# Kernel optimization log

Hardware: AMD Instinct MI355X
Metric: run time of the kernel (lower is better)

Reference implementation:

```python
import jax, jax.numpy as jnp
import numpy as np

N = 50000       # nodes
E = 800000      # edges (avg degree 16)
D_IN = 128      # input_dim
H = 256         # hidden_dim
Z = H // 2      # 128, latent / conv3-4 width
D_OUT = 64      # output_dim


def _glorot(key, shape):
    fan_in, fan_out = shape
    lim = float(np.sqrt(6.0 / (fan_in + fan_out)))
    return jax.random.uniform(key, shape, jnp.float32, -lim, lim)


def setup_inputs() -> dict:
    key = jax.random.key(0)
    ks = jax.random.split(key, 16)
    inp = {
        "x": jax.random.uniform(ks[0], (N, D_IN), jnp.float32),
        "edge_index": jax.random.randint(ks[1], (2, E), 0, N, jnp.int32),
        "epsilon": jax.random.normal(ks[2], (N, Z), jnp.float32),
        # SAGEConv params: Wl (neighbor/aggr path, with bias), Wr (root path, no bias)
        "Wl1": _glorot(ks[3], (D_IN, H)), "bl1": jnp.zeros((H,), jnp.float32), "Wr1": _glorot(ks[4], (D_IN, H)),
        "Wl2": _glorot(ks[5], (H, H)),    "bl2": jnp.zeros((H,), jnp.float32), "Wr2": _glorot(ks[6], (H, H)),
        "Wl3": _glorot(ks[7], (Z, Z)),    "bl3": jnp.zeros((Z,), jnp.float32), "Wr3": _glorot(ks[8], (Z, Z)),
        "Wl4": _glorot(ks[9], (Z, Z)),    "bl4": jnp.zeros((Z,), jnp.float32), "Wr4": _glorot(ks[10], (Z, Z)),
        "W_lin": _glorot(ks[11], (Z, D_OUT)), "b_lin": jnp.zeros((D_OUT,), jnp.float32),
    }
    return inp


def _sage_conv(x, src, dst, Wl, bl, Wr):
    # PyG SAGEConv (mean aggr): out = lin_l(mean_{j in N(i)} x_j) + lin_r(x_i)
    msg = x[src]                                             # [E, d] gather
    agg = jax.ops.segment_sum(msg, dst, num_segments=N)      # [N, d]
    cnt = jax.ops.segment_sum(jnp.ones((src.shape[0],), x.dtype), dst, num_segments=N)
    mean = agg / jnp.maximum(cnt, 1.0)[:, None]
    return mean @ Wl + bl + x @ Wr


def reference(x, edge_index, epsilon,
              Wl1, bl1, Wr1, Wl2, bl2, Wr2,
              Wl3, bl3, Wr3, Wl4, bl4, Wr4,
              W_lin, b_lin):
    src, dst = edge_index[0], edge_index[1]
    h = x / 1000.0 - 0.5
    h = jnp.sin(_sage_conv(h, src, dst, Wl1, bl1, Wr1))      # [N, H]
    h = _sage_conv(h, src, dst, Wl2, bl2, Wr2)               # [N, H]
    mean = h[:, :Z]
    log_var = h[:, Z:]
    z = mean + jnp.exp(log_var) * epsilon                    # reparameterize
    h = jax.nn.relu(_sage_conv(z, src, dst, Wl3, bl3, Wr3))
    h = jax.nn.relu(_sage_conv(h, src, dst, Wl4, bl4, Wr4))
    out = jax.nn.sigmoid(h @ W_lin + b_lin) * 1000.0
    return out, mean, log_var
```

## Files before the change

kernel.cpp:

```cpp
#include <hip/hip_runtime.h>
#include <hip/hip_bf16.h>

#define N_NODES 50000
#define E_EDGES 800000

using u16 = unsigned short;
typedef short bf8 __attribute__((ext_vector_type(8)));
typedef float f32x4 __attribute__((ext_vector_type(4)));

__device__ __forceinline__ float bf2f(u16 h) {
    union { unsigned u; float f; } v;
    v.u = ((unsigned)h) << 16;
    return v.f;
}
__device__ __forceinline__ u16 f2bf(float f) {
    union { float f; unsigned u; } v;
    v.f = f;
    unsigned r = v.u + 0x7FFF + ((v.u >> 16) & 1);
    return (u16)(r >> 16);
}

struct WtArgs {
    const float* src[9];
    u16* dst[9];
    int K[9];
    int N[9];
};

__global__ __launch_bounds__(256) void k_wpack(WtArgs a) {
    int wi = blockIdx.y;
    int K = a.K[wi], NC = a.N[wi];
    int KS = K / 32;
    int chunks = (NC / 16) * KS * 64;
    for (int c = blockIdx.x * 256 + threadIdx.x; c < chunks;
         c += gridDim.x * 256) {
        int l = c & 63;
        int rest = c >> 6;
        int ks = rest % KS, gni = rest / KS;
        int n = gni * 16 + (l & 15);
        int kb = ks * 32 + (l >> 4) * 8;
        u16 outv[8];
#pragma unroll
        for (int j = 0; j < 8; ++j)
            outv[j] = f2bf(a.src[wi][(size_t)(kb + j) * NC + n]);
        *(bf8*)&a.dst[wi][(size_t)c * 8] = *(bf8*)outv;
    }
}

__global__ __launch_bounds__(256) void k_prep(const float* __restrict__ x,
                                              u16* __restrict__ h0) {
    int total = N_NODES * 128 / 4;
    for (int i = blockIdx.x * 256 + threadIdx.x; i < total;
         i += gridDim.x * 256) {
        float4 v = *(const float4*)(x + (size_t)i * 4);
        ushort4 o;
        o.x = f2bf(v.x * 0.001f - 0.5f);
        o.y = f2bf(v.y * 0.001f - 0.5f);
        o.z = f2bf(v.z * 0.001f - 0.5f);
        o.w = f2bf(v.w * 0.001f - 0.5f);
        *(ushort4*)(h0 + (size_t)i * 4) = o;
    }
}

__global__ void k_count(const int* __restrict__ dst, int* __restrict__ deg) {
    for (int i = blockIdx.x * blockDim.x + threadIdx.x; i < E_EDGES;
         i += gridDim.x * blockDim.x)
        atomicAdd(&deg[dst[i]], 1);
}

#define SCAN_B 49

__global__ __launch_bounds__(1024) void k_scan1(const int* __restrict__ deg,
                                                int* __restrict__ bsum) {
    __shared__ int sm[1024];
    int i = blockIdx.x * 1024 + threadIdx.x;
    sm[threadIdx.x] = (i < N_NODES) ? deg[i] : 0;
    __syncthreads();
    for (int ofs = 512; ofs > 0; ofs >>= 1) {
        if (threadIdx.x < ofs) sm[threadIdx.x] += sm[threadIdx.x + ofs];
        __syncthreads();
    }
    if (threadIdx.x == 0) bsum[blockIdx.x] = sm[0];
}

__global__ void k_scan2(const int* __restrict__ bsum, int* __restrict__ bofs) {
    int l = threadIdx.x;
    int v = (l < SCAN_B) ? bsum[l] : 0;
    int orig = v;
    for (int d = 1; d < 64; d <<= 1) {
        int u = __shfl_up(v, d, 64);
        if (l >= d) v += u;
    }
    if (l < SCAN_B) bofs[l] = v - orig;
}

__global__ __launch_bounds__(1024) void k_scan3(const int* __restrict__ deg,
                                                const int* __restrict__ bofs,
                                                int* __restrict__ rowptr,
                                                float* __restrict__ dinv) {
    __shared__ int sm[1024];
    int i = blockIdx.x * 1024 + threadIdx.x;
    int d = (i < N_NODES) ? deg[i] : 0;
    sm[threadIdx.x] = d;
    __syncthreads();
    for (int ofs = 1; ofs < 1024; ofs <<= 1) {
        int u = (threadIdx.x >= (unsigned)ofs) ? sm[threadIdx.x - ofs] : 0;
        __syncthreads();
        sm[threadIdx.x] += u;
        __syncthreads();
    }
    if (i < N_NODES) {
        int incl = sm[threadIdx.x] + bofs[blockIdx.x];
        rowptr[i] = incl - d;
        dinv[i] = 1.0f / fmaxf((float)d, 1.0f);
        if (i == N_NODES - 1) rowptr[N_NODES] = incl;
    }
}

__global__ void k_fill(const int* __restrict__ src, const int* __restrict__ dst,
                       const int* __restrict__ rowptr, int* __restrict__ cursor,
                       int* __restrict__ colidx) {
    for (int i = blockIdx.x * blockDim.x + threadIdx.x; i < E_EDGES;
         i += gridDim.x * blockDim.x) {
        int d = dst[i];
        int pos = rowptr[d] + atomicAdd(&cursor[d], 1);
        colidx[pos] = src[i];
    }
}

template <int D>
__global__ __launch_bounds__(256) void k_aggregate(
    const u16* __restrict__ h, const int* __restrict__ rowptr,
    const int* __restrict__ colidx, const float* __restrict__ dinv,
    u16* __restrict__ mean) {
    constexpr int VA = D / 16;
    int node = (int)((blockIdx.x * 256 + threadIdx.x) >> 6);
    int lane = threadIdx.x & 63;
    if (node >= N_NODES) return;
    int sub = lane >> 4, lr = lane & 15;
    int beg = rowptr[node], end = rowptr[node + 1];
    float acc[VA] = {};
    int e = beg + sub;
    for (; e + 4 < end; e += 8) {
        int s0 = colidx[e];
        int s1 = colidx[e + 4];
        const u16* p0 = h + (size_t)s0 * D + lr * VA;
        const u16* p1 = h + (size_t)s1 * D + lr * VA;
        bf8 r0 = *(const bf8*)p0;
        bf8 r1 = *(const bf8*)p1;
        if (VA == 16) {
            bf8 r0b = *(const bf8*)(p0 + 8);
            bf8 r1b = *(const bf8*)(p1 + 8);
#pragma unroll
            for (int j = 0; j < 8; ++j) {
                acc[j] += bf2f((u16)r0[j]) + bf2f((u16)r1[j]);
                acc[8 + j] += bf2f((u16)r0b[j]) + bf2f((u16)r1b[j]);
            }
        } else {
#pragma unroll
            for (int j = 0; j < 8; ++j)
                acc[j] += bf2f((u16)r0[j]) + bf2f((u16)r1[j]);
        }
    }
    for (; e < end; e += 4) {
        int s = colidx[e];
        const u16* row = h + (size_t)s * D + lr * VA;
        bf8 r0 = *(const bf8*)row;
#pragma unroll
        for (int j = 0; j < 8; ++j) acc[j] += bf2f((u16)r0[j]);
        if (VA == 16) {
            bf8 r1 = *(const bf8*)(row + 8);
#pragma unroll
            for (int j = 0; j < 8; ++j) acc[8 + j] += bf2f((u16)r1[j]);
        }
    }
#pragma unroll
    for (int j = 0; j < VA; ++j) {
        acc[j] += __shfl_xor(acc[j], 16);
        acc[j] += __shfl_xor(acc[j], 32);
    }
    if (sub == 0) {
        float inv = dinv[node];
        u16 outv[VA];
#pragma unroll
        for (int j = 0; j < VA; ++j) outv[j] = f2bf(acc[j] * inv);
        u16* o = mean + (size_t)node * D + lr * VA;
        *(bf8*)o = *(bf8*)&outv[0];
        if (VA == 16) *(bf8*)(o + 8) = *(bf8*)&outv[8];
    }
}

enum { ACT_NONE = 0, ACT_SIN = 1, ACT_RELU = 2, ACT_SIGMOID1000 = 3, ACT_VAE = 4 };

template <int K, int NCB, int NC, int YS, int ACT, bool OUT_F32, bool TWO_PASS>
__global__ __launch_bounds__(512) void k_gemm(
    const u16* __restrict__ A1, const u16* __restrict__ Wp1,
    const u16* __restrict__ A2, const u16* __restrict__ Wp2,
    const float* __restrict__ bias, void* __restrict__ Cout,
    float* __restrict__ out_mean, float* __restrict__ out_lv,
    const float* __restrict__ eps) {
    constexpr int M = N_NODES;
    constexpr int NG = NCB / 16;
    constexpr int KS = K / 32;
    constexpr int CHUNKS = NG * KS * 64;
    constexpr int GX = (M / 16 + 7) / 8;
    constexpr int NWG = ((GX * YS + 7) / 8) * 8;
    constexpr int CPX = NWG / 8;
    extern __shared__ char smem[];
    u16* Bs = (u16*)smem;

    const int bid = blockIdx.x;
    const int wid = (bid & 7) * CPX + (bid >> 3);
    const int x = wid / YS;
    const int y = wid % YS;
    if (x >= GX) return;

    const int t = threadIdx.x;
    const int lane = t & 63;
    const int wave = t >> 6;
    const int lr = lane & 15;
    const int sub = lane >> 4;
    const int row0 = (x * 8 + wave) * 16;
    const int arow = row0 + lr;
    const bool rowOK = arow < M;

    auto mapGroup = [&](int ni) {
        if (ACT == ACT_VAE)
            return ni < NG / 2 ? y * (NG / 2) + ni
                               : (NC / 32) + y * (NG / 2) + (ni - NG / 2);
        return y * NG + ni;
    };

    f32x4 acc[NG];
#pragma unroll
    for (int i = 0; i < NG; ++i) acc[i] = (f32x4){0.f, 0.f, 0.f, 0.f};

    auto stageW = [&](const u16* __restrict__ Wp) {
#pragma unroll
        for (int i = 0; i < CHUNKS / 512; ++i) {
            int c = t + i * 512;
            int l = c & 63;
            int ks = (c >> 6) % KS;
            int ni = c / (64 * KS);
            size_t gsrc = ((size_t)mapGroup(ni) * KS + ks) * 64 + l;
            *(bf8*)&Bs[(size_t)c * 8] = *(const bf8*)(Wp + gsrc * 8);
        }
    };

    auto pass = [&](const u16* __restrict__ A, const u16* __restrict__ Wp) {
        stageW(Wp);
        __syncthreads();
        const u16* ap = A + (size_t)arow * K + sub * 8;
#pragma unroll
        for (int ks = 0; ks < KS; ++ks) {
            bf8 a = {0, 0, 0, 0, 0, 0, 0, 0};
            if (rowOK) a = *(const bf8*)(ap + ks * 32);
#pragma unroll
            for (int ni = 0; ni < NG; ++ni) {
                bf8 b = *(const bf8*)&Bs[(((size_t)ni * KS + ks) * 64 + lane) * 8];
                acc[ni] =
                    __builtin_amdgcn_mfma_f32_16x16x32_bf16(a, b, acc[ni], 0, 0, 0);
            }
        }
        __syncthreads();
    };

    pass(A1, Wp1);
    if (TWO_PASS) pass(A2, Wp2);

    if (ACT == ACT_VAE) {
#pragma unroll
        for (int ni = 0; ni < NG / 2; ++ni) {
            int colm = y * (NCB / 2) + ni * 16 + lr;
            float bm = bias[colm];
            float bl = bias[colm + 128];
#pragma unroll
            for (int r = 0; r < 4; ++r) {
                int row = row0 + sub * 4 + r;
                if (row >= M) continue;
                float mv = acc[ni][r] + bm;
                float lv = acc[ni + NG / 2][r] + bl;
                size_t o = (size_t)row * 128 + colm;
                out_mean[o] = mv;
                out_lv[o] = lv;
                ((u16*)Cout)[o] = f2bf(mv + __expf(lv) * eps[o]);
            }
        }
    } else {
#pragma unroll
        for (int ni = 0; ni < NG; ++ni) {
            int col = y * NCB + ni * 16 + lr;
            float bv = bias[col];
#pragma unroll
            for (int r = 0; r < 4; ++r) {
                int row = row0 + sub * 4 + r;
                if (row >= M) continue;
                float v = acc[ni][r] + bv;
                if (ACT == ACT_SIN) v = __sinf(v);
                else if (ACT == ACT_RELU) v = fmaxf(v, 0.f);
                else if (ACT == ACT_SIGMOID1000) v = 1000.f / (1.f + __expf(-v));
                if (OUT_F32)
                    ((float*)Cout)[(size_t)row * NC + col] = v;
                else
                    ((u16*)Cout)[(size_t)row * NC + col] = f2bf(v);
            }
        }
    }
}

extern "C" void kernel_launch(void* const* d_in, const int* in_sizes, int n_in,
                              void* d_out, int out_size, void* d_ws,
                              size_t ws_size, hipStream_t stream) {
    const int N = N_NODES;
    const float* x = (const float*)d_in[0];
    const int* ei = (const int*)d_in[1];
    const float* eps = (const float*)d_in[2];
    const float* Wl1 = (const float*)d_in[3];
    const float* bl1 = (const float*)d_in[4];
    const float* Wr1 = (const float*)d_in[5];
    const float* Wl2 = (const float*)d_in[6];
    const float* bl2 = (const float*)d_in[7];
    const float* Wr2 = (const float*)d_in[8];
    const float* Wl3 = (const float*)d_in[9];
    const float* bl3 = (const float*)d_in[10];
    const float* Wr3 = (const float*)d_in[11];
    const float* Wl4 = (const float*)d_in[12];
    const float* bl4 = (const float*)d_in[13];
    const float* Wr4 = (const float*)d_in[14];
    const float* W_lin = (const float*)d_in[15];
    const float* b_lin = (const float*)d_in[16];

    const int* src = ei;
    const int* dst = ei + E_EDGES;

    char* w = (char*)d_ws;
    auto alloc = [&](size_t b) {
        void* p = (void*)w;
        w += (b + 255) & ~(size_t)255;
        return p;
    };
    int* deg = (int*)alloc((size_t)N * 4);
    int* rowptr = (int*)alloc((size_t)(N + 1) * 4);
    int* cursor = (int*)alloc((size_t)N * 4);
    int* colidx = (int*)alloc((size_t)E_EDGES * 4);
    float* dinv = (float*)alloc((size_t)N * 4);
    int* bsum = (int*)alloc(64 * 4);
    int* bofs = (int*)alloc(64 * 4);
    u16* hbA = (u16*)alloc((size_t)N * 256 * 2);
    u16* hbB = (u16*)alloc((size_t)N * 256 * 2);
    u16* hbC = (u16*)alloc((size_t)N * 256 * 2);
    static const int wK[9] = {128, 128, 256, 256, 128, 128, 128, 128, 128};
    static const int wN[9] = {256, 256, 256, 256, 128, 128, 128, 128, 64};
    u16* Wt[9];
    for (int i = 0; i < 9; ++i) Wt[i] = (u16*)alloc((size_t)wK[i] * wN[i] * 2);

    float* out_final = (float*)d_out;
    float* out_mean = out_final + (size_t)N * 64;
    float* out_lv = out_mean + (size_t)N * 128;

    hipMemsetAsync(deg, 0, (size_t)N * 4, stream);
    hipMemsetAsync(cursor, 0, (size_t)N * 4, stream);

    WtArgs wa;
    const float* wsrc[9] = {Wl1, Wr1, Wl2, Wr2, Wl3, Wr3, Wl4, Wr4, W_lin};
    for (int i = 0; i < 9; ++i) {
        wa.src[i] = wsrc[i];
        wa.dst[i] = Wt[i];
        wa.K[i] = wK[i];
        wa.N[i] = wN[i];
    }
    k_wpack<<<dim3(32, 9), 256, 0, stream>>>(wa);

    k_prep<<<2048, 256, 0, stream>>>(x, hbA);
    k_count<<<3125, 256, 0, stream>>>(dst, deg);
    k_scan1<<<SCAN_B, 1024, 0, stream>>>(deg, bsum);
    k_scan2<<<1, 64, 0, stream>>>(bsum, bofs);
    k_scan3<<<SCAN_B, 1024, 0, stream>>>(deg, bofs, rowptr, dinv);
    k_fill<<<3125, 256, 0, stream>>>(src, dst, rowptr, cursor, colidx);

    const int aggBlocks = (N * 64 + 255) / 256;
    auto nwg = [](int YS) { return ((391 * YS + 7) / 8) * 8; };
    auto shm = [](int NCB, int K) { return (size_t)NCB * K * 2; };

    k_aggregate<128><<<aggBlocks, 256, 0, stream>>>(hbA, rowptr, colidx, dinv,
                                                    hbB);
    k_gemm<128, 128, 256, 2, ACT_SIN, false, true>
        <<<nwg(2), 512, shm(128, 128), stream>>>(hbB, Wt[0], hbA, Wt[1], bl1,
                                                 hbC, nullptr, nullptr, nullptr);

    k_aggregate<256><<<aggBlocks, 256, 0, stream>>>(hbC, rowptr, colidx, dinv,
                                                    hbB);
    k_gemm<256, 64, 256, 4, ACT_VAE, false, true>
        <<<nwg(4), 512, shm(64, 256), stream>>>(hbB, Wt[2], hbC, Wt[3], bl2,
                                                hbA, out_mean, out_lv, eps);

    k_aggregate<128><<<aggBlocks, 256, 0, stream>>>(hbA, rowptr, colidx, dinv,
                                                    hbB);
    k_gemm<128, 64, 128, 2, ACT_RELU, false, true>
        <<<nwg(2), 512, shm(64, 128), stream>>>(hbB, Wt[4], hbA, Wt[5], bl3,
                                                hbC, nullptr, nullptr, nullptr);

    k_aggregate<128><<<aggBlocks, 256, 0, stream>>>(hbC, rowptr, colidx, dinv,
                                                    hbB);
    k_gemm<128, 64, 128, 2, ACT_RELU, false, true>
        <<<nwg(2), 512, shm(64, 128), stream>>>(hbB, Wt[6], hbC, Wt[7], bl4,
                                                hbA, nullptr, nullptr, nullptr);

    k_gemm<128, 32, 64, 2, ACT_SIGMOID1000, true, false>
        <<<nwg(2), 512, shm(32, 128), stream>>>(hbA, Wt[8], nullptr, nullptr,
                                                b_lin, out_final, nullptr,
                                                nullptr, nullptr);
}
```

Measured before the change: 371.4 us.

## Compute two row tiles per wave in GEMM and unroll aggregation gather by four

The GEMM kernel now has each wave compute two 16-row MFMA tiles that share the same B fragments from LDS, halving the workgroup count and reusing staged weights across more rows. The first layer's GEMM is retiled to 64-column blocks with four column groups. The aggregation loop processes four neighbors per iteration instead of two, putting more independent gathers in flight. These add register pressure from doubled accumulators and may reduce occupancy.

Result: slower. 379.5 us (+2.2%).

```diff
diff --git a/kernel.cpp b/kernel.cpp
--- a/kernel.cpp
+++ b/kernel.cpp
@@ -141,25 +141,28 @@
     int beg = rowptr[node], end = rowptr[node + 1];
     float acc[VA] = {};
     int e = beg + sub;
-    for (; e + 4 < end; e += 8) {
-        int s0 = colidx[e];
-        int s1 = colidx[e + 4];
-        const u16* p0 = h + (size_t)s0 * D + lr * VA;
-        const u16* p1 = h + (size_t)s1 * D + lr * VA;
+    for (; e + 12 < end; e += 16) {
+        const u16* p0 = h + (size_t)colidx[e] * D + lr * VA;
+        const u16* p1 = h + (size_t)colidx[e + 4] * D + lr * VA;
+        const u16* p2 = h + (size_t)colidx[e + 8] * D + lr * VA;
+        const u16* p3 = h + (size_t)colidx[e + 12] * D + lr * VA;
         bf8 r0 = *(const bf8*)p0;
         bf8 r1 = *(const bf8*)p1;
+        bf8 r2 = *(const bf8*)p2;
+        bf8 r3 = *(const bf8*)p3;
+#pragma unroll
+        for (int j = 0; j < 8; ++j)
+            acc[j] += (bf2f((u16)r0[j]) + bf2f((u16)r1[j])) +
+                      (bf2f((u16)r2[j]) + bf2f((u16)r3[j]));
         if (VA == 16) {
-            bf8 r0b = *(const bf8*)(p0 + 8);
-            bf8 r1b = *(const bf8*)(p1 + 8);
-#pragma unroll
-            for (int j = 0; j < 8; ++j) {
-                acc[j] += bf2f((u16)r0[j]) + bf2f((u16)r1[j]);
-                acc[8 + j] += bf2f((u16)r0b[j]) + bf2f((u16)r1b[j]);
-            }
-        } else {
+            bf8 s0 = *(const bf8*)(p0 + 8);
+            bf8 s1 = *(const bf8*)(p1 + 8);
+            bf8 s2 = *(const bf8*)(p2 + 8);
+            bf8 s3 = *(const bf8*)(p3 + 8);
 #pragma unroll
             for (int j = 0; j < 8; ++j)
-                acc[j] += bf2f((u16)r0[j]) + bf2f((u16)r1[j]);
+                acc[8 + j] += (bf2f((u16)s0[j]) + bf2f((u16)s1[j])) +
+                              (bf2f((u16)s2[j]) + bf2f((u16)s3[j]));
         }
     }
     for (; e < end; e += 4) {
@@ -203,7 +206,7 @@
     constexpr int NG = NCB / 16;
     constexpr int KS = K / 32;
     constexpr int CHUNKS = NG * KS * 64;
-    constexpr int GX = (M / 16 + 7) / 8;
+    constexpr int GX = (M + 255) / 256;
     constexpr int NWG = ((GX * YS + 7) / 8) * 8;
     constexpr int CPX = NWG / 8;
     extern __shared__ char smem[];
@@ -220,9 +223,11 @@
     const int wave = t >> 6;
     const int lr = lane & 15;
     const int sub = lane >> 4;
-    const int row0 = (x * 8 + wave) * 16;
-    const int arow = row0 + lr;
-    const bool rowOK = arow < M;
+    const int wrow0 = (x * 8 + wave) * 32;
+    const int arow0 = wrow0 + lr;
+    const int arow1 = wrow0 + 16 + lr;
+    const bool ok0 = arow0 < M;
+    const bool ok1 = arow1 < M;
 
     auto mapGroup = [&](int ni) {
         if (ACT == ACT_VAE)
@@ -231,9 +236,12 @@
         return y * NG + ni;
     };
 
-    f32x4 acc[NG];
-#pragma unroll
-    for (int i = 0; i < NG; ++i) acc[i] = (f32x4){0.f, 0.f, 0.f, 0.f};
+    f32x4 acc0[NG], acc1[NG];
+#pragma unroll
+    for (int i = 0; i < NG; ++i) {
+        acc0[i] = (f32x4){0.f, 0.f, 0.f, 0.f};
+        acc1[i] = (f32x4){0.f, 0.f, 0.f, 0.f};
+    }
 
     auto stageW = [&](const u16* __restrict__ Wp) {
 #pragma unroll
@@ -250,16 +258,21 @@
     auto pass = [&](const u16* __restrict__ A, const u16* __restrict__ Wp) {
         stageW(Wp);
         __syncthreads();
-        const u16* ap = A + (size_t)arow * K + sub * 8;
+        const u16* ap0 = A + (size_t)arow0 * K + sub * 8;
+        const u16* ap1 = A + (size_t)arow1 * K + sub * 8;
 #pragma unroll
         for (int ks = 0; ks < KS; ++ks) {
-            bf8 a = {0, 0, 0, 0, 0, 0, 0, 0};
-            if (rowOK) a = *(const bf8*)(ap + ks * 32);
+            bf8 a0 = {0, 0, 0, 0, 0, 0, 0, 0};
+            bf8 a1 = {0, 0, 0, 0, 0, 0, 0, 0};
+            if (ok0) a0 = *(const bf8*)(ap0 + ks * 32);
+            if (ok1) a1 = *(const bf8*)(ap1 + ks * 32);
 #pragma unroll
             for (int ni = 0; ni < NG; ++ni) {
                 bf8 b = *(const bf8*)&Bs[(((size_t)ni * KS + ks) * 64 + lane) * 8];
-                acc[ni] =
-                    __builtin_amdgcn_mfma_f32_16x16x32_bf16(a, b, acc[ni], 0, 0, 0);
+                acc0[ni] =
+                    __builtin_amdgcn_mfma_f32_16x16x32_bf16(a0, b, acc0[ni], 0, 0, 0);
+                acc1[ni] =
+                    __builtin_amdgcn_mfma_f32_16x16x32_bf16(a1, b, acc1[ni], 0, 0, 0);
             }
         }
         __syncthreads();
@@ -275,15 +288,19 @@
             float bm = bias[colm];
             float bl = bias[colm + 128];
 #pragma unroll
-            for (int r = 0; r < 4; ++r) {
-                int row = row0 + sub * 4 + r;
-                if (row >= M) continue;
-                float mv = acc[ni][r] + bm;
-                float lv = acc[ni + NG / 2][r] + bl;
-                size_t o = (size_t)row * 128 + colm;
-                out_mean[o] = mv;
-                out_lv[o] = lv;
-                ((u16*)Cout)[o] = f2bf(mv + __expf(lv) * eps[o]);
+            for (int s = 0; s < 2; ++s) {
+#pragma unroll
+                for (int r = 0; r < 4; ++r) {
+                    int row = wrow0 + s * 16 + sub * 4 + r;
+                    if (row >= M) continue;
+                    float mv = (s ? acc1[ni][r] : acc0[ni][r]) + bm;
+                    float lv =
+                        (s ? acc1[ni + NG / 2][r] : acc0[ni + NG / 2][r]) + bl;
+                    size_t o = (size_t)row * 128 + colm;
+                    out_mean[o] = mv;
+                    out_lv[o] = lv;
+                    ((u16*)Cout)[o] = f2bf(mv + __expf(lv) * eps[o]);
+                }
             }
         }
     } else {
@@ -292,17 +309,21 @@
             int col = y * NCB + ni * 16 + lr;
             float bv = bias[col];
 #pragma unroll
-            for (int r = 0; r < 4; ++r) {
-                int row = row0 + sub * 4 + r;
-                if (row >= M) continue;
-                float v = acc[ni][r] + bv;
-                if (ACT == ACT_SIN) v = __sinf(v);
-                else if (ACT == ACT_RELU) v = fmaxf(v, 0.f);
-                else if (ACT == ACT_SIGMOID1000) v = 1000.f / (1.f + __expf(-v));
-                if (OUT_F32)
-                    ((float*)Cout)[(size_t)row * NC + col] = v;
-                else
-                    ((u16*)Cout)[(size_t)row * NC + col] = f2bf(v);
+            for (int s = 0; s < 2; ++s) {
+#pragma unroll
+                for (int r = 0; r < 4; ++r) {
+                    int row = wrow0 + s * 16 + sub * 4 + r;
+                    if (row >= M) continue;
+                    float v = (s ? acc1[ni][r] : acc0[ni][r]) + bv;
+                    if (ACT == ACT_SIN) v = __sinf(v);
+                    else if (ACT == ACT_RELU) v = fmaxf(v, 0.f);
+                    else if (ACT == ACT_SIGMOID1000)
+                        v = 1000.f / (1.f + __expf(-v));
+                    if (OUT_F32)
+                        ((float*)Cout)[(size_t)row * NC + col] = v;
+                    else
+                        ((u16*)Cout)[(size_t)row * NC + col] = f2bf(v);
+                }
             }
         }
     }
@@ -379,14 +400,14 @@
     k_fill<<<3125, 256, 0, stream>>>(src, dst, rowptr, cursor, colidx);
 
     const int aggBlocks = (N * 64 + 255) / 256;
-    auto nwg = [](int YS) { return ((391 * YS + 7) / 8) * 8; };
+    auto nwg = [](int YS) { return ((196 * YS + 7) / 8) * 8; };
     auto shm = [](int NCB, int K) { return (size_t)NCB * K * 2; };
 
     k_aggregate<128><<<aggBlocks, 256, 0, stream>>>(hbA, rowptr, colidx, dinv,
                                                     hbB);
-    k_gemm<128, 128, 256, 2, ACT_SIN, false, true>
-        <<<nwg(2), 512, shm(128, 128), stream>>>(hbB, Wt[0], hbA, Wt[1], bl1,
-                                                 hbC, nullptr, nullptr, nullptr);
+    k_gemm<128, 64, 256, 4, ACT_SIN, false, true>
+        <<<nwg(4), 512, shm(64, 128), stream>>>(hbB, Wt[0], hbA, Wt[1], bl1,
+                                                hbC, nullptr, nullptr, nullptr);
 
     k_aggregate<256><<<aggBlocks, 256, 0, stream>>>(hbC, rowptr, colidx, dinv,
                                                     hbB);
```

## Stage both weight passes via async global-to-LDS loads and prefetch A fragments

Applied to the files above, without the earlier changes.

The GEMM kernel now loads both weight matrices into shared memory up front with global_load_lds direct-to-LDS transfers and a single barrier, instead of two staged passes through registers each with its own syncs. The K loop is merged across the two passes and software-prefetches the next A fragment. The VAE epsilon values are loaded before the main loop, and layer 1 switches to a narrower column split with twice as many workgroups. Doubling LDS per block may reduce occupancy.

After: 367.3 us. Within noise of the previous version (-1.1%).

```diff
diff --git a/kernel.cpp b/kernel.cpp
--- a/kernel.cpp
+++ b/kernel.cpp
@@ -19,6 +19,11 @@
     unsigned r = v.u + 0x7FFF + ((v.u >> 16) & 1);
     return (u16)(r >> 16);
 }
+
+#define GLOAD_LDS16(gsrc, ldst)                                            \
+    __builtin_amdgcn_global_load_lds(                                      \
+        (const __attribute__((address_space(1))) void*)(gsrc),             \
+        (__attribute__((address_space(3))) void*)(ldst), 16, 0, 0)
 
 struct WtArgs {
     const float* src[9];
@@ -201,8 +206,9 @@
     const float* __restrict__ eps) {
     constexpr int M = N_NODES;
     constexpr int NG = NCB / 16;
-    constexpr int KS = K / 32;
-    constexpr int CHUNKS = NG * KS * 64;
+    constexpr int KS1 = K / 32;
+    constexpr int KST = TWO_PASS ? 2 * KS1 : KS1;
+    constexpr int CH1 = NG * KS1 * 64;
     constexpr int GX = (M / 16 + 7) / 8;
     constexpr int NWG = ((GX * YS + 7) / 8) * 8;
     constexpr int CPX = NWG / 8;
@@ -231,42 +237,78 @@
         return y * NG + ni;
     };
 
+    {
+#pragma unroll
+        for (int i = 0; i < CH1 / 512; ++i) {
+            int c = t + i * 512;
+            int ks = (c >> 6) % KS1;
+            int ni = c / (64 * KS1);
+            const u16* gsrc =
+                Wp1 + (((size_t)mapGroup(ni) * KS1 + ks) * 64 + lane) * 8;
+            u16* ldst = Bs + ((size_t)(i * 512 + wave * 64)) * 8;
+            GLOAD_LDS16(gsrc, ldst);
+        }
+        if (TWO_PASS) {
+#pragma unroll
+            for (int i = 0; i < CH1 / 512; ++i) {
+                int c = t + i * 512;
+                int ks = (c >> 6) % KS1;
+                int ni = c / (64 * KS1);
+                const u16* gsrc =
+                    Wp2 + (((size_t)mapGroup(ni) * KS1 + ks) * 64 + lane) * 8;
+                u16* ldst = Bs + ((size_t)(CH1 + i * 512 + wave * 64)) * 8;
+                GLOAD_LDS16(gsrc, ldst);
+            }
+        }
+    }
+
+    float epsv[ACT == ACT_VAE ? 8 : 1];
+    if (ACT == ACT_VAE) {
+#pragma unroll
+        for (int ni = 0; ni < NG / 2; ++ni) {
+#pragma unroll
+            for (int r = 0; r < 4; ++r) {
+                int row = row0 + sub * 4 + r;
+                int colm = y * (NCB / 2) + ni * 16 + lr;
+                epsv[ni * 4 + r] =
+                    (row < M) ? eps[(size_t)row * 128 + colm] : 0.f;
+            }
+        }
+    }
+
     f32x4 acc[NG];
 #pragma unroll
     for (int i = 0; i < NG; ++i) acc[i] = (f32x4){0.f, 0.f, 0.f, 0.f};
 
-    auto stageW = [&](const u16* __restrict__ Wp) {
-#pragma unroll
-        for (int i = 0; i < CHUNKS / 512; ++i) {
-            int c = t + i * 512;
-            int l = c & 63;
-            int ks = (c >> 6) % KS;
-            int ni = c / (64 * KS);
-            size_t gsrc = ((size_t)mapGroup(ni) * KS + ks) * 64 + l;
-            *(bf8*)&Bs[(size_t)c * 8] = *(const bf8*)(Wp + gsrc * 8);
-        }
+    auto aptr = [&](int ks) {
+        return (ks < KS1 ? A1 + (size_t)arow * K + ks * 32
+                         : A2 + (size_t)arow * K + (ks - KS1) * 32) +
+               sub * 8;
     };
 
-    auto pass = [&](const u16* __restrict__ A, const u16* __restrict__ Wp) {
-        stageW(Wp);
-        __syncthreads();
-        const u16* ap = A + (size_t)arow * K + sub * 8;
-#pragma unroll
-        for (int ks = 0; ks < KS; ++ks) {
-            bf8 a = {0, 0, 0, 0, 0, 0, 0, 0};
-            if (rowOK) a = *(const bf8*)(ap + ks * 32);
-#pragma unroll
-            for (int ni = 0; ni < NG; ++ni) {
-                bf8 b = *(const bf8*)&Bs[(((size_t)ni * KS + ks) * 64 + lane) * 8];
-                acc[ni] =
-                    __builtin_amdgcn_mfma_f32_16x16x32_bf16(a, b, acc[ni], 0, 0, 0);
-            }
-        }
-        __syncthreads();
-    };
-
-    pass(A1, Wp1);
-    if (TWO_PASS) pass(A2, Wp2);
+    __syncthreads();
+
+    bf8 acur = {0, 0, 0, 0, 0, 0, 0, 0};
+    if (rowOK) acur = *(const bf8*)aptr(0);
+#pragma unroll
+    for (int ks = 0; ks < KST; ++ks) {
+        bf8 anext = {0, 0, 0, 0, 0, 0, 0, 0};
+        if (ks + 1 < KST && rowOK) anext = *(const bf8*)aptr(ks + 1);
+#pragma unroll
+        for (int ni = 0; ni < NG; ++ni) {
+            bf8 b = *(const bf8*)&Bs[(((size_t)ks * NG + 0) * 0 +
+                                      ((ks < KS1)
+                                           ? (((size_t)ni * KS1 + ks) * 64)
+                                           : ((size_t)CH1 +
+                                              ((size_t)ni * KS1 + (ks - KS1)) *
+                                                  64)) +
+                                      lane) *
+                                     8];
+            acc[ni] =
+                __builtin_amdgcn_mfma_f32_16x16x32_bf16(acur, b, acc[ni], 0, 0, 0);
+        }
+        acur = anext;
+    }
 
     if (ACT == ACT_VAE) {
 #pragma unroll
@@ -283,7 +325,7 @@
                 size_t o = (size_t)row * 128 + colm;
                 out_mean[o] = mv;
                 out_lv[o] = lv;
-                ((u16*)Cout)[o] = f2bf(mv + __expf(lv) * eps[o]);
+                ((u16*)Cout)[o] = f2bf(mv + __expf(lv) * epsv[ni * 4 + r]);
             }
         }
     } else {
@@ -380,30 +422,30 @@
 
     const int aggBlocks = (N * 64 + 255) / 256;
     auto nwg = [](int YS) { return ((391 * YS + 7) / 8) * 8; };
-    auto shm = [](int NCB, int K) { return (size_t)NCB * K * 2; };
+    auto shm = [](int NCB, int Ktot) { return (size_t)NCB * Ktot * 2; };
 
     k_aggregate<128><<<aggBlocks, 256, 0, stream>>>(hbA, rowptr, colidx, dinv,
                                                     hbB);
-    k_gemm<128, 128, 256, 2, ACT_SIN, false, true>
-        <<<nwg(2), 512, shm(128, 128), stream>>>(hbB, Wt[0], hbA, Wt[1], bl1,
-                                                 hbC, nullptr, nullptr, nullptr);
+    k_gemm<128, 64, 256, 4, ACT_SIN, false, true>
+        <<<nwg(4), 512, shm(64, 256), stream>>>(hbB, Wt[0], hbA, Wt[1], bl1,
+                                                hbC, nullptr, nullptr, nullptr);
 
     k_aggregate<256><<<aggBlocks, 256, 0, stream>>>(hbC, rowptr, colidx, dinv,
                                                     hbB);
     k_gemm<256, 64, 256, 4, ACT_VAE, false, true>
-        <<<nwg(4), 512, shm(64, 256), stream>>>(hbB, Wt[2], hbC, Wt[3], bl2,
+        <<<nwg(4), 512, shm(64, 512), stream>>>(hbB, Wt[2], hbC, Wt[3], bl2,
                                                 hbA, out_mean, out_lv, eps);
 
     k_aggregate<128><<<aggBlocks, 256, 0, stream>>>(hbA, rowptr, colidx, dinv,
                                                     hbB);
     k_gemm<128, 64, 128, 2, ACT_RELU, false, true>
-        <<<nwg(2), 512, shm(64, 128), stream>>>(hbB, Wt[4], hbA, Wt[5], bl3,
+        <<<nwg(2), 512, shm(64, 256), stream>>>(hbB, Wt[4], hbA, Wt[5], bl3,
                                                 hbC, nullptr, nullptr, nullptr);
 
     k_aggregate<128><<<aggBlocks, 256, 0, stream>>>(hbC, rowptr, colidx, dinv,
                                                     hbB);
     k_gemm<128, 64, 128, 2, ACT_RELU, false, true>
-        <<<nwg(2), 512, shm(64, 128), stream>>>(hbB, Wt[6], hbC, Wt[7], bl4,
+        <<<nwg(2), 512, shm(64, 256), stream>>>(hbB, Wt[6], hbC, Wt[7], bl4,
                                                 hbA, nullptr, nullptr, nullptr);
 
     k_gemm<128, 32, 64, 2, ACT_SIGMOID1000, true, false>
```

## Co-schedule root-path GEMM with neighbor aggregation in one heterogeneous launch

Applied to the files above, without the earlier changes.

Each SAGE layer's root-path GEMM (x @ Wr) now runs inside the aggregation kernel. Every R-th block does a GEMM tile and writes a bf16 partial S, while the other blocks do the mean aggregation, so compute-bound MFMA work can overlap the memory-bound gather. The second kernel then does only the mean @ Wl GEMM and adds S in its epilogue. Weight staging also switches to global_load_lds direct-to-LDS copies, and the A operand gets a one-step register prefetch. The costs are an extra round trip through a bf16 S buffer, an added rounding step for the root term, and block-interleaving ratios that were tuned by hand.

Result: slower. 384.3 us (+3.5%).

```diff
diff --git a/kernel.cpp b/kernel.cpp
--- a/kernel.cpp
+++ b/kernel.cpp
@@ -19,6 +19,11 @@
     unsigned r = v.u + 0x7FFF + ((v.u >> 16) & 1);
     return (u16)(r >> 16);
 }
+
+#define GLOAD_LDS16(gsrc, ldst)                                            \
+    __builtin_amdgcn_global_load_lds(                                      \
+        (const __attribute__((address_space(1))) void*)(gsrc),             \
+        (__attribute__((address_space(3))) void*)(ldst), 16, 0, 0)
 
 struct WtArgs {
     const float* src[9];
@@ -128,24 +133,98 @@
     }
 }
 
-template <int D>
-__global__ __launch_bounds__(256) void k_aggregate(
-    const u16* __restrict__ h, const int* __restrict__ rowptr,
-    const int* __restrict__ colidx, const float* __restrict__ dinv,
-    u16* __restrict__ mean) {
-    constexpr int VA = D / 16;
-    int node = (int)((blockIdx.x * 256 + threadIdx.x) >> 6);
-    int lane = threadIdx.x & 63;
-    if (node >= N_NODES) return;
-    int sub = lane >> 4, lr = lane & 15;
+template <int K, int NCB, int NC, int YS, int R>
+__global__ __launch_bounds__(512) void k_conv_a(
+    const u16* __restrict__ H, const u16* __restrict__ Wp,
+    const int* __restrict__ rowptr, const int* __restrict__ colidx,
+    const float* __restrict__ dinv, u16* __restrict__ meanOut,
+    u16* __restrict__ S) {
+    constexpr int M = N_NODES;
+    constexpr int NG = NCB / 16;
+    constexpr int KS = K / 32;
+    constexpr int CH = NG * KS * 64;
+    constexpr int GX = (M / 16 + 7) / 8;
+    constexpr int GEMM_B = ((GX * YS + 7) / 8) * 8;
+    constexpr int CPX = GEMM_B / 8;
+    extern __shared__ char smem[];
+    u16* Bs = (u16*)smem;
+
+    const int bid = blockIdx.x;
+    const int t = threadIdx.x;
+    const int lane = t & 63;
+    const int wave = t >> 6;
+    const int lr = lane & 15;
+    const int sub = lane >> 4;
+
+    if (bid % R == R - 1) {
+        const int gid = bid / R;
+        const int wid = (gid & 7) * CPX + (gid >> 3);
+        const int x = wid / YS;
+        const int y = wid % YS;
+        if (x >= GX) return;
+        const int row0 = (x * 8 + wave) * 16;
+        const int arow = row0 + lr;
+        const bool rowOK = arow < M;
+
+#pragma unroll
+        for (int i = 0; i < CH / 512; ++i) {
+            int c = t + i * 512;
+            int ks = (c >> 6) % KS;
+            int ni = c / (64 * KS);
+            const u16* gsrc =
+                Wp + (((size_t)(y * NG + ni) * KS + ks) * 64 + lane) * 8;
+            u16* ldst = Bs + ((size_t)(i * 512 + wave * 64)) * 8;
+            GLOAD_LDS16(gsrc, ldst);
+        }
+
+        f32x4 acc[NG];
+#pragma unroll
+        for (int i = 0; i < NG; ++i) acc[i] = (f32x4){0.f, 0.f, 0.f, 0.f};
+
+        const u16* ap = H + (size_t)arow * K + sub * 8;
+        __syncthreads();
+
+        bf8 acur = {0, 0, 0, 0, 0, 0, 0, 0};
+        if (rowOK) acur = *(const bf8*)ap;
+#pragma unroll
+        for (int ks = 0; ks < KS; ++ks) {
+            bf8 anext = {0, 0, 0, 0, 0, 0, 0, 0};
+            if (ks + 1 < KS && rowOK) anext = *(const bf8*)(ap + (ks + 1) * 32);
+#pragma unroll
+            for (int ni = 0; ni < NG; ++ni) {
+                bf8 b =
+                    *(const bf8*)&Bs[(((size_t)ni * KS + ks) * 64 + lane) * 8];
+                acc[ni] = __builtin_amdgcn_mfma_f32_16x16x32_bf16(acur, b,
+                                                                  acc[ni], 0, 0, 0);
+            }
+            acur = anext;
+        }
+
+#pragma unroll
+        for (int ni = 0; ni < NG; ++ni) {
+            int col = y * NCB + ni * 16 + lr;
+#pragma unroll
+            for (int r = 0; r < 4; ++r) {
+                int row = row0 + sub * 4 + r;
+                if (row >= M) continue;
+                S[(size_t)row * NC + col] = f2bf(acc[ni][r]);
+            }
+        }
+        return;
+    }
+
+    constexpr int VA = K / 16;
+    const int agg_id = bid - bid / R;
+    const int node = agg_id * 8 + wave;
+    if (node >= M) return;
     int beg = rowptr[node], end = rowptr[node + 1];
     float acc[VA] = {};
     int e = beg + sub;
     for (; e + 4 < end; e += 8) {
         int s0 = colidx[e];
         int s1 = colidx[e + 4];
-        const u16* p0 = h + (size_t)s0 * D + lr * VA;
-        const u16* p1 = h + (size_t)s1 * D + lr * VA;
+        const u16* p0 = H + (size_t)s0 * K + lr * VA;
+        const u16* p1 = H + (size_t)s1 * K + lr * VA;
         bf8 r0 = *(const bf8*)p0;
         bf8 r1 = *(const bf8*)p1;
         if (VA == 16) {
@@ -164,7 +243,7 @@
     }
     for (; e < end; e += 4) {
         int s = colidx[e];
-        const u16* row = h + (size_t)s * D + lr * VA;
+        const u16* row = H + (size_t)s * K + lr * VA;
         bf8 r0 = *(const bf8*)row;
 #pragma unroll
         for (int j = 0; j < 8; ++j) acc[j] += bf2f((u16)r0[j]);
@@ -184,7 +263,7 @@
         u16 outv[VA];
 #pragma unroll
         for (int j = 0; j < VA; ++j) outv[j] = f2bf(acc[j] * inv);
-        u16* o = mean + (size_t)node * D + lr * VA;
+        u16* o = meanOut + (size_t)node * K + lr * VA;
         *(bf8*)o = *(bf8*)&outv[0];
         if (VA == 16) *(bf8*)(o + 8) = *(bf8*)&outv[8];
     }
@@ -192,20 +271,19 @@
 
 enum { ACT_NONE = 0, ACT_SIN = 1, ACT_RELU = 2, ACT_SIGMOID1000 = 3, ACT_VAE = 4 };
 
-template <int K, int NCB, int NC, int YS, int ACT, bool OUT_F32, bool TWO_PASS>
-__global__ __launch_bounds__(512) void k_gemm(
-    const u16* __restrict__ A1, const u16* __restrict__ Wp1,
-    const u16* __restrict__ A2, const u16* __restrict__ Wp2,
-    const float* __restrict__ bias, void* __restrict__ Cout,
-    float* __restrict__ out_mean, float* __restrict__ out_lv,
-    const float* __restrict__ eps) {
+template <int K, int NCB, int NC, int YS, int ACT, bool OUT_F32, bool ADD_S>
+__global__ __launch_bounds__(512) void k_conv_b(
+    const u16* __restrict__ A, const u16* __restrict__ Wp,
+    const u16* __restrict__ S, const float* __restrict__ bias,
+    void* __restrict__ Cout, float* __restrict__ out_mean,
+    float* __restrict__ out_lv, const float* __restrict__ eps) {
     constexpr int M = N_NODES;
     constexpr int NG = NCB / 16;
     constexpr int KS = K / 32;
-    constexpr int CHUNKS = NG * KS * 64;
+    constexpr int CH = NG * KS * 64;
     constexpr int GX = (M / 16 + 7) / 8;
-    constexpr int NWG = ((GX * YS + 7) / 8) * 8;
-    constexpr int CPX = NWG / 8;
+    constexpr int GEMM_B = ((GX * YS + 7) / 8) * 8;
+    constexpr int CPX = GEMM_B / 8;
     extern __shared__ char smem[];
     u16* Bs = (u16*)smem;
 
@@ -231,42 +309,38 @@
         return y * NG + ni;
     };
 
+#pragma unroll
+    for (int i = 0; i < CH / 512; ++i) {
+        int c = t + i * 512;
+        int ks = (c >> 6) % KS;
+        int ni = c / (64 * KS);
+        const u16* gsrc =
+            Wp + (((size_t)mapGroup(ni) * KS + ks) * 64 + lane) * 8;
+        u16* ldst = Bs + ((size_t)(i * 512 + wave * 64)) * 8;
+        GLOAD_LDS16(gsrc, ldst);
+    }
+
     f32x4 acc[NG];
 #pragma unroll
     for (int i = 0; i < NG; ++i) acc[i] = (f32x4){0.f, 0.f, 0.f, 0.f};
 
-    auto stageW = [&](const u16* __restrict__ Wp) {
-#pragma unroll
-        for (int i = 0; i < CHUNKS / 512; ++i) {
-            int c = t + i * 512;
-            int l = c & 63;
-            int ks = (c >> 6) % KS;
-            int ni = c / (64 * KS);
-            size_t gsrc = ((size_t)mapGroup(ni) * KS + ks) * 64 + l;
-            *(bf8*)&Bs[(size_t)c * 8] = *(const bf8*)(Wp + gsrc * 8);
-        }
-    };
-
-    auto pass = [&](const u16* __restrict__ A, const u16* __restrict__ Wp) {
-        stageW(Wp);
-        __syncthreads();
-        const u16* ap = A + (size_t)arow * K + sub * 8;
-#pragma unroll
-        for (int ks = 0; ks < KS; ++ks) {
-            bf8 a = {0, 0, 0, 0, 0, 0, 0, 0};
-            if (rowOK) a = *(const bf8*)(ap + ks * 32);
-#pragma unroll
-            for (int ni = 0; ni < NG; ++ni) {
-                bf8 b = *(const bf8*)&Bs[(((size_t)ni * KS + ks) * 64 + lane) * 8];
-                acc[ni] =
-                    __builtin_amdgcn_mfma_f32_16x16x32_bf16(a, b, acc[ni], 0, 0, 0);
-            }
-        }
-        __syncthreads();
-    };
-
-    pass(A1, Wp1);
-    if (TWO_PASS) pass(A2, Wp2);
+    const u16* ap = A + (size_t)arow * K + sub * 8;
+    __syncthreads();
+
+    bf8 acur = {0, 0, 0, 0, 0, 0, 0, 0};
+    if (rowOK) acur = *(const bf8*)ap;
+#pragma unroll
+    for (int ks = 0; ks < KS; ++ks) {
+        bf8 anext = {0, 0, 0, 0, 0, 0, 0, 0};
+        if (ks + 1 < KS && rowOK) anext = *(const bf8*)(ap + (ks + 1) * 32);
+#pragma unroll
+        for (int ni = 0; ni < NG; ++ni) {
+            bf8 b = *(const bf8*)&Bs[(((size_t)ni * KS + ks) * 64 + lane) * 8];
+            acc[ni] =
+                __builtin_amdgcn_mfma_f32_16x16x32_bf16(acur, b, acc[ni], 0, 0, 0);
+        }
+        acur = anext;
+    }
 
     if (ACT == ACT_VAE) {
 #pragma unroll
@@ -278,8 +352,9 @@
             for (int r = 0; r < 4; ++r) {
                 int row = row0 + sub * 4 + r;
                 if (row >= M) continue;
-                float mv = acc[ni][r] + bm;
-                float lv = acc[ni + NG / 2][r] + bl;
+                float mv = acc[ni][r] + bm + bf2f(S[(size_t)row * NC + colm]);
+                float lv = acc[ni + NG / 2][r] + bl +
+                           bf2f(S[(size_t)row * NC + colm + 128]);
                 size_t o = (size_t)row * 128 + colm;
                 out_mean[o] = mv;
                 out_lv[o] = lv;
@@ -296,6 +371,7 @@
                 int row = row0 + sub * 4 + r;
                 if (row >= M) continue;
                 float v = acc[ni][r] + bv;
+                if (ADD_S) v += bf2f(S[(size_t)row * NC + col]);
                 if (ACT == ACT_SIN) v = __sinf(v);
                 else if (ACT == ACT_RELU) v = fmaxf(v, 0.f);
                 else if (ACT == ACT_SIGMOID1000) v = 1000.f / (1.f + __expf(-v));
@@ -349,6 +425,7 @@
     u16* hbA = (u16*)alloc((size_t)N * 256 * 2);
     u16* hbB = (u16*)alloc((size_t)N * 256 * 2);
     u16* hbC = (u16*)alloc((size_t)N * 256 * 2);
+    u16* hbS = (u16*)alloc((size_t)N * 256 * 2);
     static const int wK[9] = {128, 128, 256, 256, 128, 128, 128, 128, 128};
     static const int wN[9] = {256, 256, 256, 256, 128, 128, 128, 128, 64};
     u16* Wt[9];
@@ -378,36 +455,34 @@
     k_scan3<<<SCAN_B, 1024, 0, stream>>>(deg, bofs, rowptr, dinv);
     k_fill<<<3125, 256, 0, stream>>>(src, dst, rowptr, cursor, colidx);
 
-    const int aggBlocks = (N * 64 + 255) / 256;
-    auto nwg = [](int YS) { return ((391 * YS + 7) / 8) * 8; };
     auto shm = [](int NCB, int K) { return (size_t)NCB * K * 2; };
 
-    k_aggregate<128><<<aggBlocks, 256, 0, stream>>>(hbA, rowptr, colidx, dinv,
-                                                    hbB);
-    k_gemm<128, 128, 256, 2, ACT_SIN, false, true>
-        <<<nwg(2), 512, shm(128, 128), stream>>>(hbB, Wt[0], hbA, Wt[1], bl1,
-                                                 hbC, nullptr, nullptr, nullptr);
-
-    k_aggregate<256><<<aggBlocks, 256, 0, stream>>>(hbC, rowptr, colidx, dinv,
-                                                    hbB);
-    k_gemm<256, 64, 256, 4, ACT_VAE, false, true>
-        <<<nwg(4), 512, shm(64, 256), stream>>>(hbB, Wt[2], hbC, Wt[3], bl2,
-                                                hbA, out_mean, out_lv, eps);
-
-    k_aggregate<128><<<aggBlocks, 256, 0, stream>>>(hbA, rowptr, colidx, dinv,
-                                                    hbB);
-    k_gemm<128, 64, 128, 2, ACT_RELU, false, true>
-        <<<nwg(2), 512, shm(64, 128), stream>>>(hbB, Wt[4], hbA, Wt[5], bl3,
-                                                hbC, nullptr, nullptr, nullptr);
-
-    k_aggregate<128><<<aggBlocks, 256, 0, stream>>>(hbC, rowptr, colidx, dinv,
-                                                    hbB);
-    k_gemm<128, 64, 128, 2, ACT_RELU, false, true>
-        <<<nwg(2), 512, shm(64, 128), stream>>>(hbB, Wt[6], hbC, Wt[7], bl4,
-                                                hbA, nullptr, nullptr, nullptr);
-
-    k_gemm<128, 32, 64, 2, ACT_SIGMOID1000, true, false>
-        <<<nwg(2), 512, shm(32, 128), stream>>>(hbA, Wt[8], nullptr, nullptr,
-                                                b_lin, out_final, nullptr,
-                                                nullptr, nullptr);
-}
+    k_conv_a<128, 64, 256, 4, 5><<<1568 * 5, 512, shm(64, 128), stream>>>(
+        hbA, Wt[1], rowptr, colidx, dinv, hbB, hbS);
+    k_conv_b<128, 64, 256, 4, ACT_SIN, false, true>
+        <<<1568, 512, shm(64, 128), stream>>>(hbB, Wt[0], hbS, bl1, hbC,
+                                              nullptr, nullptr, nullptr);
+
+    k_conv_a<256, 64, 256, 4, 5><<<1568 * 5, 512, shm(64, 256), stream>>>(
+        hbC, Wt[3], rowptr, colidx, dinv, hbB, hbS);
+    k_conv_b<256, 64, 256, 4, ACT_VAE, false, true>
+        <<<1568, 512, shm(64, 256), stream>>>(hbB, Wt[2], hbS, bl2, hbA,
+                                              out_mean, out_lv, eps);
+
+    k_conv_a<128, 64, 128, 2, 9><<<784 * 9, 512, shm(64, 128), stream>>>(
+        hbA, Wt[5], rowptr, colidx, dinv, hbB, hbS);
+    k_conv_b<128, 64, 128, 2, ACT_RELU, false, true>
+        <<<784, 512, shm(64, 128), stream>>>(hbB, Wt[4], hbS, bl3, hbC,
+                                             nullptr, nullptr, nullptr);
+
+    k_conv_a<128, 64, 128, 2, 9><<<784 * 9, 512, shm(64, 128), stream>>>(
+        hbC, Wt[7], rowptr, colidx, dinv, hbB, hbS);
+    k_conv_b<128, 64, 128, 2, ACT_RELU, false, true>
+        <<<784, 512, shm(64, 128), stream>>>(hbB, Wt[6], hbS, bl4, hbA,
+                                             nullptr, nullptr, nullptr);
+
+    k_conv_b<128, 32, 64, 2, ACT_SIGMOID1000, true, false>
+        <<<784, 512, shm(32, 128), stream>>>(hbA, Wt[8], nullptr, b_lin,
+                                             out_final, nullptr, nullptr,
+                                             nullptr);
+}
```
